# Performance work log

Measured on AMD Instinct MI355X. Metric: run time of the kernel, lower is better.

Reference implementation:

```python
import jax, jax.numpy as jnp
import numpy as np

B, L, D = 16, 2048, 128
NEG = -1.0e9


def setup_inputs() -> dict:
    key = jax.random.key(0)
    kq, kk, kv, km = jax.random.split(key, 4)
    Q = jax.random.normal(kq, (B, L, D), dtype=jnp.float32)
    K = jax.random.normal(kk, (B, L, D), dtype=jnp.float32)
    V = jax.random.normal(kv, (B, L, D), dtype=jnp.float32)
    scale = jnp.float32(1.0 / np.sqrt(D))
    # original code masks rows where (mask + 1) == 0, i.e. mask == -1
    mask = jnp.where(jax.random.uniform(km, (B, L)) < 0.1, -1, 0).astype(jnp.int32)
    return {"Q": Q, "K": K, "V": V, "scale": scale, "mask": mask}


def reference(Q, K, V, scale, mask):
    # attention = Q @ K^T * scale  -> [B, Lq, Lk]
    att = jnp.einsum("bqd,bkd->bqk", Q, K) * scale
    # mask[b, i] broadcast over the key dim j (row-wise masking, as in the
    # original unsqueeze(-1).expand pattern with square attention)
    row_masked = (mask + 1) == 0  # [B, L]
    att = jnp.where(row_masked[:, :, None], NEG, att)
    att = jax.nn.softmax(att, axis=-1)
    context = jnp.einsum("bqk,bkd->bqd", att, V)
    return context
```

## Files before the change

kernel.cpp:

```cpp
#include <hip/hip_runtime.h>


#define NB 16
#define LL 2048
#define DD 128
#define LOG2E 1.44269504f

typedef __attribute__((ext_vector_type(8))) short short8;
typedef __attribute__((ext_vector_type(16))) float f32x16;

__device__ __forceinline__ float wexp2(float x) {
  float r; asm("v_exp_f32 %0, %1" : "=v"(r) : "v"(x)); return r;
}
__device__ __forceinline__ unsigned cvtpk(float lo, float hi) {
  unsigned r; asm("v_cvt_pk_bf16_f32 %0, %1, %2" : "=v"(r) : "v"(lo), "v"(hi)); return r;
}
__device__ __forceinline__ void gll16(const void* g, const void* l) {
  __builtin_amdgcn_global_load_lds(
      (const __attribute__((address_space(1))) unsigned*)g,
      (__attribute__((address_space(3))) unsigned*)l, 16, 0, 0);
}

__global__ void prep_qk(const float* __restrict__ Q, const float* __restrict__ K,
                        const float* __restrict__ scale, const int* __restrict__ mask,
                        short* __restrict__ Qb, short* __restrict__ Kb) {
  int bid = blockIdx.x;
  int g = ((bid & 2047) << 8) + threadIdx.x;
  if (bid < 2048) {
    float sc = scale[0];
    float msc = (mask[g >> 4] == -1) ? 0.f : sc;
    const float4* qp = (const float4*)Q + (size_t)g * 2;
    float4 a = qp[0], c = qp[1];
    ((uint4*)Qb)[g] = make_uint4(cvtpk(a.x * msc, a.y * msc), cvtpk(a.z * msc, a.w * msc),
                                 cvtpk(c.x * msc, c.y * msc), cvtpk(c.z * msc, c.w * msc));
  } else {
    const float4* kp = (const float4*)K + (size_t)g * 2;
    float4 a = kp[0], c = kp[1];
    ((uint4*)Kb)[g] = make_uint4(cvtpk(a.x, a.y), cvtpk(a.z, a.w),
                                 cvtpk(c.x, c.y), cvtpk(c.z, c.w));
  }
}

__global__ void prep_vt(const float* __restrict__ V, short* __restrict__ Vt) {
  __shared__ short lds[64 * 130];
  int b = blockIdx.x >> 5;
  int t0 = (blockIdx.x & 31) * 64;
  int t = threadIdx.x;
  #pragma unroll
  for (int i = 0; i < 8; ++i) {
    int c = t + i * 256;
    int kv = c >> 5, ds = (c & 31) * 4;
    float4 v = *(const float4*)(V + ((size_t)(b * LL + t0 + kv) * DD + ds));
    unsigned* dst = (unsigned*)(&lds[kv * 130 + ds]);
    dst[0] = cvtpk(v.x, v.y);
    dst[1] = cvtpk(v.z, v.w);
  }
  __syncthreads();
  int d = t >> 1, hf = t & 1;
  unsigned dw[16];
  #pragma unroll
  for (int i = 0; i < 16; ++i) {
    int kv = hf * 32 + i * 2;
    unsigned lo16 = (unsigned short)lds[kv * 130 + d];
    unsigned hi16 = (unsigned short)lds[(kv + 1) * 130 + d];
    dw[i] = lo16 | (hi16 << 16);
  }
  short* orow = Vt + (size_t)(b * DD + d) * LL + t0 + hf * 32;
  #pragma unroll
  for (int i = 0; i < 4; ++i)
    ((uint4*)orow)[i] = make_uint4(dw[4 * i], dw[4 * i + 1], dw[4 * i + 2], dw[4 * i + 3]);
}

__global__ __launch_bounds__(512, 2) void attn_main(
    const short* __restrict__ Qb, const short* __restrict__ Kb,
    const short* __restrict__ Vt, float* __restrict__ Out) {
  __shared__ __align__(16) char smem[67584];
  const int tid = threadIdx.x;
  const int w = tid >> 6, l = tid & 63, lo = l & 31, hi = l >> 5;
  const int qg = w & 3, kvh = w >> 2;

  int lg = (blockIdx.x & 7) * 32 + (blockIdx.x >> 3);
  int b = lg >> 4;
  int q0 = (lg & 15) * 128 + qg * 32;

  short8 qf[8];
  const short* qp = Qb + (size_t)(b * LL + q0 + lo) * DD;
  #pragma unroll
  for (int dc = 0; dc < 8; ++dc)
    qf[dc] = *(const short8*)(qp + dc * 16 + hi * 8);

  const char* kgb = (const char*)(Kb + (size_t)b * (LL * DD));
  const char* vgb = (const char*)(Vt + (size_t)b * (LL * DD));

#define STAGE(bi_, kv0_) do { \
    char* kbuf = smem + (bi_) * 16384; \
    char* vbuf = smem + 32768 + (bi_) * 16384; \
    _Pragma("unroll") \
    for (int i = 0; i < 2; ++i) { \
      int c = w * 2 + i; \
      int kr = c * 4 + (l >> 4); \
      int kc = ((l & 15) << 4) ^ ((kr & 15) << 4); \
      gll16(kgb + (size_t)((kv0_) + kr) * 256 + kc, kbuf + c * 1024); \
      int vr = c * 8 + (l >> 3); \
      int vc = ((l & 7) << 4) ^ ((vr & 7) << 4); \
      gll16(vgb + (size_t)vr * 4096 + (size_t)(kv0_) * 2 + vc, vbuf + c * 1024); \
    } \
  } while (0)

  STAGE(0, 0);
  __syncthreads();

  f32x16 oacc[4];
  #pragma unroll
  for (int dt = 0; dt < 4; ++dt)
    #pragma unroll
    for (int r = 0; r < 16; ++r) oacc[dt][r] = 0.f;
  float m = -INFINITY, lsum = 0.f;

  const int swzk = (lo & 15) << 4;
  const int swzv = (lo & 7) << 4;

  #pragma unroll 1
  for (int tt = 0; tt < 32; ++tt) {
    int cur = tt & 1;
    if (tt < 31) STAGE(cur ^ 1, (tt + 1) * 64);
    const char* kb = smem + cur * 16384;
    const char* vb = smem + 32768 + cur * 16384;

    f32x16 acc;
    #pragma unroll
    for (int r = 0; r < 16; ++r) acc[r] = 0.f;
    const char* krow = kb + (kvh * 32 + lo) * 256;
    #pragma unroll
    for (int dc = 0; dc < 8; ++dc) {
      short8 kf = *(const short8*)(krow + ((dc * 32 + hi * 16) ^ swzk));
      acc = __builtin_amdgcn_mfma_f32_32x32x16_bf16(kf, qf[dc], acc, 0, 0, 0);
    }
    float tmax = acc[0];
    #pragma unroll
    for (int r = 1; r < 16; ++r) tmax = fmaxf(tmax, acc[r]);
    #pragma unroll
    for (int off = 1; off < 64; off <<= 1) tmax = fmaxf(tmax, __shfl_xor(tmax, off));
    if (tmax > m + 8.0f) {
      float al = wexp2((m - tmax) * LOG2E);
      m = tmax;
      lsum *= al;
      #pragma unroll
      for (int dt = 0; dt < 4; ++dt)
        #pragma unroll
        for (int r = 0; r < 16; ++r) oacc[dt][r] *= al;
    }
    float ps = 0.f;
    #pragma unroll
    for (int r = 0; r < 16; ++r) {
      float p = wexp2((acc[r] - m) * LOG2E);
      acc[r] = p; ps += p;
    }
    lsum += ps;
    short8 pa[2];
    #pragma unroll
    for (int ks = 0; ks < 2; ++ks) {
      unsigned a0 = cvtpk(acc[ks * 8 + 0], acc[ks * 8 + 1]);
      unsigned b0 = cvtpk(acc[ks * 8 + 4], acc[ks * 8 + 5]);
      unsigned c0 = cvtpk(acc[ks * 8 + 2], acc[ks * 8 + 3]);
      unsigned d0 = cvtpk(acc[ks * 8 + 6], acc[ks * 8 + 7]);
      asm volatile("v_permlane32_swap_b32 %0, %1" : "+v"(a0), "+v"(b0));
      asm volatile("v_permlane32_swap_b32 %0, %1" : "+v"(c0), "+v"(d0));
      union { unsigned u[4]; short8 s; } pu;
      pu.u[0] = a0; pu.u[1] = c0; pu.u[2] = b0; pu.u[3] = d0;
      pa[ks] = pu.s;
    }
    #pragma unroll
    for (int dt = 0; dt < 4; ++dt) {
      const char* vrow = vb + (dt * 32 + lo) * 128;
      #pragma unroll
      for (int ks = 0; ks < 2; ++ks) {
        short8 vf = *(const short8*)(vrow + ((kvh * 64 + ks * 32 + hi * 16) ^ swzv));
        oacc[dt] = __builtin_amdgcn_mfma_f32_32x32x16_bf16(pa[ks], vf, oacc[dt], 0, 0, 0);
      }
    }
    __syncthreads();
  }
#undef STAGE

  float* lsb = (float*)(smem + 65536);
  float* mb  = (float*)(smem + 66560);
  float* rdb = (float*)(smem + 66576);
  if (kvh == 1) {
    #pragma unroll
    for (int dt = 0; dt < 4; ++dt)
      #pragma unroll
      for (int i = 0; i < 4; ++i)
        *(float4*)(smem + qg * 16384 + l * 256 + ((dt * 64 + i * 16) ^ ((l & 15) << 4))) =
            make_float4(oacc[dt][4 * i], oacc[dt][4 * i + 1],
                        oacc[dt][4 * i + 2], oacc[dt][4 * i + 3]);
    lsb[qg * 64 + l] = lsum;
    if (l == 0) mb[qg] = m;
  }
  __syncthreads();
  if (kvh == 0) {
    float mp = mb[qg];
    float M = fmaxf(m, mp);
    float aa = wexp2((m - M) * LOG2E), ab = wexp2((mp - M) * LOG2E);
    float ls = lsum * aa + lsb[qg * 64 + l] * ab;
    float lt = ls + __shfl_xor(ls, 32);
    float rd = 1.0f / lt;
    if (l < 32) rdb[qg * 32 + l] = rd;
    #pragma unroll
    for (int dt = 0; dt < 4; ++dt)
      #pragma unroll
      for (int i = 0; i < 4; ++i) {
        float4 p = *(const float4*)(smem + qg * 16384 + l * 256 +
                                    ((dt * 64 + i * 16) ^ ((l & 15) << 4)));
        oacc[dt][4 * i + 0] = oacc[dt][4 * i + 0] * aa + p.x * ab;
        oacc[dt][4 * i + 1] = oacc[dt][4 * i + 1] * aa + p.y * ab;
        oacc[dt][4 * i + 2] = oacc[dt][4 * i + 2] * aa + p.z * ab;
        oacc[dt][4 * i + 3] = oacc[dt][4 * i + 3] * aa + p.w * ab;
      }
    #pragma unroll
    for (int r = 0; r < 16; ++r) {
      int cr = (r & 3) + 8 * (r >> 2) + 4 * hi;
      float rr = rdb[qg * 32 + cr];
      float* op = Out + (size_t)(b * LL + q0 + cr) * DD + lo;
      #pragma unroll
      for (int dt = 0; dt < 4; ++dt)
        op[dt * 32] = oacc[dt][r] * rr;
    }
  }
}

extern "C" void kernel_launch(void* const* d_in, const int* in_sizes, int n_in,
                              void* d_out, int out_size, void* d_ws, size_t ws_size,
                              hipStream_t stream) {
  const float* Q = (const float*)d_in[0];
  const float* K = (const float*)d_in[1];
  const float* V = (const float*)d_in[2];
  const float* scale = (const float*)d_in[3];
  const int* mask = (const int*)d_in[4];
  float* out = (float*)d_out;

  const size_t tensor_elems = (size_t)NB * LL * DD;
  const size_t need = 3 * tensor_elems * sizeof(short);
  if (ws_size < need) return;

  short* Qb = (short*)d_ws;
  short* Kb = Qb + tensor_elems;
  short* Vtp = Kb + tensor_elems;

  hipLaunchKernelGGL(prep_qk, dim3(4096), dim3(256), 0, stream, Q, K, scale, mask, Qb, Kb);
  hipLaunchKernelGGL(prep_vt, dim3(512), dim3(256), 0, stream, V, Vtp);
  hipLaunchKernelGGL(attn_main, dim3(256), dim3(512), 0, stream, Qb, Kb, Vtp, out);
}
```

Measured before the change: 71.21 us.

## Split KV loop across two wave phases with 1024-thread blocks and two-level merge

```diff
diff --git a/kernel.cpp b/kernel.cpp
--- a/kernel.cpp
+++ b/kernel.cpp
@@ -71,13 +71,13 @@
     ((uint4*)orow)[i] = make_uint4(dw[4 * i], dw[4 * i + 1], dw[4 * i + 2], dw[4 * i + 3]);
 }
 
-__global__ __launch_bounds__(512, 2) void attn_main(
+__global__ __launch_bounds__(1024, 4) void attn_main(
     const short* __restrict__ Qb, const short* __restrict__ Kb,
     const short* __restrict__ Vt, float* __restrict__ Out) {
-  __shared__ __align__(16) char smem[67584];
+  __shared__ __align__(16) char smem[135744];
   const int tid = threadIdx.x;
   const int w = tid >> 6, l = tid & 63, lo = l & 31, hi = l >> 5;
-  const int qg = w & 3, kvh = w >> 2;
+  const int qg = w & 3, kvh = (w >> 2) & 1, ph = w >> 3;
 
   int lg = (blockIdx.x & 7) * 32 + (blockIdx.x >> 3);
   int b = lg >> 4;
@@ -92,22 +92,18 @@
   const char* kgb = (const char*)(Kb + (size_t)b * (LL * DD));
   const char* vgb = (const char*)(Vt + (size_t)b * (LL * DD));
 
+  const int kr = tid >> 4;
+  const int koff = kr * 256 + (((tid & 15) << 4) ^ ((kr & 15) << 4));
+  const int vr = tid >> 3;
+  const size_t voff = (size_t)vr * 4096 + (((tid & 7) << 4) ^ ((vr & 7) << 4));
+
 #define STAGE(bi_, kv0_) do { \
-    char* kbuf = smem + (bi_) * 16384; \
-    char* vbuf = smem + 32768 + (bi_) * 16384; \
-    _Pragma("unroll") \
-    for (int i = 0; i < 2; ++i) { \
-      int c = w * 2 + i; \
-      int kr = c * 4 + (l >> 4); \
-      int kc = ((l & 15) << 4) ^ ((kr & 15) << 4); \
-      gll16(kgb + (size_t)((kv0_) + kr) * 256 + kc, kbuf + c * 1024); \
-      int vr = c * 8 + (l >> 3); \
-      int vc = ((l & 7) << 4) ^ ((vr & 7) << 4); \
-      gll16(vgb + (size_t)vr * 4096 + (size_t)(kv0_) * 2 + vc, vbuf + c * 1024); \
-    } \
+    gll16(kgb + (size_t)(kv0_) * 256 + koff, smem + (bi_) * 16384 + tid * 16); \
+    gll16(vgb + (size_t)(kv0_) * 2 + voff, smem + 65536 + (bi_) * 16384 + tid * 16); \
   } while (0)
 
   STAGE(0, 0);
+  STAGE(1, 64);
   __syncthreads();
 
   f32x16 oacc[4];
@@ -115,17 +111,20 @@
   for (int dt = 0; dt < 4; ++dt)
     #pragma unroll
     for (int r = 0; r < 16; ++r) oacc[dt][r] = 0.f;
-  float m = -INFINITY, lsum = 0.f;
+  float m = -INFINITY, lsum = 0.f, nm = -INFINITY;
 
   const int swzk = (lo & 15) << 4;
   const int swzv = (lo & 7) << 4;
 
   #pragma unroll 1
-  for (int tt = 0; tt < 32; ++tt) {
-    int cur = tt & 1;
-    if (tt < 31) STAGE(cur ^ 1, (tt + 1) * 64);
-    const char* kb = smem + cur * 16384;
-    const char* vb = smem + 32768 + cur * 16384;
+  for (int it = 0; it < 16; ++it) {
+    int pb = (it & 1) * 2;
+    if (it < 15) {
+      STAGE(pb ^ 2, (2 * it + 2) * 64);
+      STAGE((pb ^ 2) | 1, (2 * it + 3) * 64);
+    }
+    const char* kb = smem + (pb + ph) * 16384;
+    const char* vb = smem + 65536 + (pb + ph) * 16384;
 
     f32x16 acc;
     #pragma unroll
@@ -136,14 +135,16 @@
       short8 kf = *(const short8*)(krow + ((dc * 32 + hi * 16) ^ swzk));
       acc = __builtin_amdgcn_mfma_f32_32x32x16_bf16(kf, qf[dc], acc, 0, 0, 0);
     }
-    float tmax = acc[0];
-    #pragma unroll
-    for (int r = 1; r < 16; ++r) tmax = fmaxf(tmax, acc[r]);
+    float tmax = fmaxf(fmaxf(fmaxf(acc[0], acc[1]), fmaxf(acc[2], acc[3])),
+                       fmaxf(fmaxf(acc[4], acc[5]), fmaxf(acc[6], acc[7])));
+    float t2 = fmaxf(fmaxf(fmaxf(acc[8], acc[9]), fmaxf(acc[10], acc[11])),
+                     fmaxf(fmaxf(acc[12], acc[13]), fmaxf(acc[14], acc[15])));
+    tmax = fmaxf(tmax, t2);
     #pragma unroll
     for (int off = 1; off < 64; off <<= 1) tmax = fmaxf(tmax, __shfl_xor(tmax, off));
     if (tmax > m + 8.0f) {
       float al = wexp2((m - tmax) * LOG2E);
-      m = tmax;
+      m = tmax; nm = -m * LOG2E;
       lsum *= al;
       #pragma unroll
       for (int dt = 0; dt < 4; ++dt)
@@ -153,7 +154,7 @@
     float ps = 0.f;
     #pragma unroll
     for (int r = 0; r < 16; ++r) {
-      float p = wexp2((acc[r] - m) * LOG2E);
+      float p = wexp2(__builtin_fmaf(acc[r], LOG2E, nm));
       acc[r] = p; ps += p;
     }
     lsum += ps;
@@ -183,40 +184,52 @@
   }
 #undef STAGE
 
-  float* lsb = (float*)(smem + 65536);
-  float* mb  = (float*)(smem + 66560);
-  float* rdb = (float*)(smem + 66576);
-  if (kvh == 1) {
-    #pragma unroll
-    for (int dt = 0; dt < 4; ++dt)
-      #pragma unroll
-      for (int i = 0; i < 4; ++i)
-        *(float4*)(smem + qg * 16384 + l * 256 + ((dt * 64 + i * 16) ^ ((l & 15) << 4))) =
-            make_float4(oacc[dt][4 * i], oacc[dt][4 * i + 1],
-                        oacc[dt][4 * i + 2], oacc[dt][4 * i + 3]);
-    lsb[qg * 64 + l] = lsum;
-    if (l == 0) mb[qg] = m;
-  }
-  __syncthreads();
-  if (kvh == 0) {
-    float mp = mb[qg];
-    float M = fmaxf(m, mp);
-    float aa = wexp2((m - M) * LOG2E), ab = wexp2((mp - M) * LOG2E);
-    float ls = lsum * aa + lsb[qg * 64 + l] * ab;
-    float lt = ls + __shfl_xor(ls, 32);
+  float* lsb = (float*)(smem + 131072);
+  float* mb  = (float*)(smem + 131072 + 4096);
+  float* rdb = (float*)(smem + 131072 + 4160);
+
+#define PUBLISH(slot_) do { \
+    char* reg_ = smem + (slot_) * 16384; \
+    _Pragma("unroll") \
+    for (int dt = 0; dt < 4; ++dt) \
+      _Pragma("unroll") \
+      for (int i = 0; i < 4; ++i) \
+        *(float4*)(reg_ + l * 256 + ((dt * 64 + i * 16) ^ ((l & 15) << 4))) = \
+            make_float4(oacc[dt][4 * i], oacc[dt][4 * i + 1], \
+                        oacc[dt][4 * i + 2], oacc[dt][4 * i + 3]); \
+    lsb[(slot_) * 64 + l] = lsum; \
+    if (l == 0) mb[slot_] = m; \
+  } while (0)
+
+#define MERGE(slot_) do { \
+    char* reg_ = smem + (slot_) * 16384; \
+    float mp = mb[slot_]; \
+    float M = fmaxf(m, mp); \
+    float aa = wexp2((m - M) * LOG2E), ab = wexp2((mp - M) * LOG2E); \
+    m = M; \
+    lsum = lsum * aa + lsb[(slot_) * 64 + l] * ab; \
+    _Pragma("unroll") \
+    for (int dt = 0; dt < 4; ++dt) \
+      _Pragma("unroll") \
+      for (int i = 0; i < 4; ++i) { \
+        float4 p = *(const float4*)(reg_ + l * 256 + ((dt * 64 + i * 16) ^ ((l & 15) << 4))); \
+        oacc[dt][4 * i + 0] = oacc[dt][4 * i + 0] * aa + p.x * ab; \
+        oacc[dt][4 * i + 1] = oacc[dt][4 * i + 1] * aa + p.y * ab; \
+        oacc[dt][4 * i + 2] = oacc[dt][4 * i + 2] * aa + p.z * ab; \
+        oacc[dt][4 * i + 3] = oacc[dt][4 * i + 3] * aa + p.w * ab; \
+      } \
+  } while (0)
+
+  if (ph == 1) PUBLISH(qg * 2 + kvh);
+  __syncthreads();
+  if (ph == 0) MERGE(qg * 2 + kvh);
+  if (ph == 0 && kvh == 1) PUBLISH(qg * 2 + 1);
+  __syncthreads();
+  if (ph == 0 && kvh == 0) {
+    MERGE(qg * 2 + 1);
+    float lt = lsum + __shfl_xor(lsum, 32);
     float rd = 1.0f / lt;
     if (l < 32) rdb[qg * 32 + l] = rd;
-    #pragma unroll
-    for (int dt = 0; dt < 4; ++dt)
-      #pragma unroll
-      for (int i = 0; i < 4; ++i) {
-        float4 p = *(const float4*)(smem + qg * 16384 + l * 256 +
-                                    ((dt * 64 + i * 16) ^ ((l & 15) << 4)));
-        oacc[dt][4 * i + 0] = oacc[dt][4 * i + 0] * aa + p.x * ab;
-        oacc[dt][4 * i + 1] = oacc[dt][4 * i + 1] * aa + p.y * ab;
-        oacc[dt][4 * i + 2] = oacc[dt][4 * i + 2] * aa + p.z * ab;
-        oacc[dt][4 * i + 3] = oacc[dt][4 * i + 3] * aa + p.w * ab;
-      }
     #pragma unroll
     for (int r = 0; r < 16; ++r) {
       int cr = (r & 3) + 8 * (r >> 2) + 4 * hi;
@@ -227,6 +240,8 @@
         op[dt * 32] = oacc[dt][r] * rr;
     }
   }
+#undef PUBLISH
+#undef MERGE
 }
 
 extern "C" void kernel_launch(void* const* d_in, const int* in_sizes, int n_in,
@@ -249,5 +264,5 @@
 
   hipLaunchKernelGGL(prep_qk, dim3(4096), dim3(256), 0, stream, Q, K, scale, mask, Qb, Kb);
   hipLaunchKernelGGL(prep_vt, dim3(512), dim3(256), 0, stream, V, Vtp);
-  hipLaunchKernelGGL(attn_main, dim3(256), dim3(512), 0, stream, Qb, Kb, Vtp, out);
-}
+  hipLaunchKernelGGL(attn_main, dim3(256), dim3(1024), 0, stream, Qb, Kb, Vtp, out);
+}
```

After: 109.2 us. 1.53x slower.
